# Performance work log

Hardware: AMD Instinct MI355X
Metric: run time of the kernel (lower is better)

## Reference

```python
import jax, jax.numpy as jnp
import numpy as np

C = 256
CQK = C // 8  # 32


def setup_inputs() -> dict:
    key = jax.random.key(0)
    ks = jax.random.split(key, 7)
    x = jax.random.normal(ks[0], (4, C, 64, 64), dtype=jnp.float32)
    s = 1.0 / np.sqrt(C)
    Wq = jax.random.normal(ks[1], (CQK, C), dtype=jnp.float32) * s
    bq = jnp.zeros((CQK,), dtype=jnp.float32)
    Wk = jax.random.normal(ks[2], (CQK, C), dtype=jnp.float32) * s
    bk = jnp.zeros((CQK,), dtype=jnp.float32)
    Wv = jax.random.normal(ks[3], (C, C), dtype=jnp.float32) * s
    bv = jnp.zeros((C,), dtype=jnp.float32)
    return {"x": x, "Wq": Wq, "bq": bq, "Wk": Wk, "bk": bk, "Wv": Wv, "bv": bv}


def reference(x, Wq, bq, Wk, bk, Wv, bv):
    B, Cc, H, W = x.shape
    xf = x.reshape(B, Cc, H * W)  # [B, C, HW]
    # 1x1 convs == per-pixel linear projections over channels
    q = jnp.einsum('oc,bcn->bno', Wq, xf) + bq          # [B, HW, C//8]
    k = jnp.einsum('oc,bcn->bon', Wk, xf) + bk[:, None]  # [B, C//8, HW]
    v = jnp.einsum('oc,bcn->bno', Wv, xf) + bv          # [B, HW, C]
    attn = jax.nn.softmax(jnp.einsum('bnd,bdm->bnm', q, k), axis=-1)  # [B, HW, HW]
    out = jnp.einsum('bnm,bmc->bnc', attn, v)           # [B, HW, C]
    return out.transpose(0, 2, 1).reshape(B, Cc, H, W)
```

## Files before the change

### kernel.cpp

```cpp
#include <hip/hip_runtime.h>
#include <hip/hip_bf16.h>


#define N_PIX 4096
#define DQK   32
#define CCH   256
#define LOG2E 1.44269504088896f

typedef __attribute__((ext_vector_type(8))) _Float16 f16x8;
typedef __attribute__((ext_vector_type(4))) _Float16 f16x4;
typedef __attribute__((ext_vector_type(2))) _Float16 f16x2;
typedef __attribute__((ext_vector_type(8))) short    bf16x8;
typedef __attribute__((ext_vector_type(4))) short    bf16x4;
typedef __attribute__((ext_vector_type(4))) float    f32x4;

__device__ inline void barrier_lds() {
    asm volatile("" ::: "memory");
    __builtin_amdgcn_s_waitcnt(0xc07f);
    __builtin_amdgcn_s_barrier();
    asm volatile("" ::: "memory");
}

__device__ inline short bf16bits(float f) {
    __hip_bfloat16 h = __float2bfloat16(f);
    return *(short*)&h;
}

__global__ __launch_bounds__(256) void wpack_kernel(
    const float* __restrict__ Wq, const float* __restrict__ Wk,
    const float* __restrict__ Wv, _Float16* __restrict__ Wp)
{
    const int tid   = threadIdx.x;
    const int wflat = blockIdx.x * 4 + (tid >> 6);
    const int lane  = tid & 63;
    const int L15   = lane & 15;
    const int quad  = lane >> 4;
    const int mt    = wflat >> 3;
    const int ks    = wflat & 7;
    const int m0    = mt * 16;

    const float* Wsrc; int row; float scale = 1.f;
    if (m0 < 32)      { Wsrc = Wq; row = m0 + L15;      scale = LOG2E; }
    else if (m0 < 64) { Wsrc = Wk; row = m0 - 32 + L15; }
    else              { Wsrc = Wv; row = m0 - 64 + L15; }

    const float* p = Wsrc + (size_t)row * 256 + ks * 32 + quad * 8;
    f16x8 h;
    #pragma unroll
    for (int j = 0; j < 8; ++j) h[j] = (_Float16)(p[j] * scale);
    *(f16x8*)(Wp + ((size_t)wflat * 64 + lane) * 8) = h;
}

__global__ __launch_bounds__(512, 4) void qkv_kernel(
    const float* __restrict__ x, const _Float16* __restrict__ Wp,
    const float* __restrict__ bq, const float* __restrict__ bk,
    const float* __restrict__ bv,
    _Float16* __restrict__ qo, _Float16* __restrict__ ko,
    __hip_bfloat16* __restrict__ vp)
{
    __shared__ alignas(16) unsigned char shraw[256 * 40 * 2];
    _Float16       (*xT)[264] = (_Float16 (*)[264])shraw;
    __hip_bfloat16 (*vst)[40] = (__hip_bfloat16 (*)[40])shraw;

    const int idx = blockIdx.x;
    const int b   = (idx & 7) >> 1;
    const int n0  = (((idx >> 3) << 1) | (idx & 1)) * 32;
    const int tid = threadIdx.x;

    {
        const float* xb = x + (size_t)b * CCH * N_PIX;
        float4 ld[2][2];
        int c2s[2], n4s[2];
        #pragma unroll
        for (int pass = 0; pass < 2; ++pass) {
            const int flat = pass * 512 + tid;
            c2s[pass] = (flat >> 3) * 2;
            n4s[pass] = (flat & 7) * 4;
            ld[pass][0] = *(const float4*)(xb + (size_t)c2s[pass]       * N_PIX + n0 + n4s[pass]);
            ld[pass][1] = *(const float4*)(xb + (size_t)(c2s[pass] + 1) * N_PIX + n0 + n4s[pass]);
        }
        #pragma unroll
        for (int pass = 0; pass < 2; ++pass) {
            const float a[4] = {ld[pass][0].x, ld[pass][0].y, ld[pass][0].z, ld[pass][0].w};
            const float c[4] = {ld[pass][1].x, ld[pass][1].y, ld[pass][1].z, ld[pass][1].w};
            #pragma unroll
            for (int i = 0; i < 4; ++i)
                *(f16x2*)(&xT[n4s[pass] + i][c2s[pass]]) =
                    (f16x2){(_Float16)a[i], (_Float16)c[i]};
        }
    }
    __syncthreads();

    const int lane = tid & 63;
    const int wid  = tid >> 6;
    const int L15  = lane & 15;
    const int quad = lane >> 4;
    const int nf   = wid & 1;
    const int mtg  = wid >> 1;

    const f32x4 fz = {0.f, 0.f, 0.f, 0.f};
    f32x4 acc[5];
    #pragma unroll
    for (int mt = 0; mt < 5; ++mt) acc[mt] = fz;

    const _Float16* wpw = Wp + ((size_t)(mtg * 5) * 8 * 64 + lane) * 8;

    #pragma unroll
    for (int ks = 0; ks < 8; ++ks) {
        const f16x8 bfr = *(const f16x8*)(&xT[nf * 16 + L15][ks * 32 + quad * 8]);
        #pragma unroll
        for (int mt = 0; mt < 5; ++mt) {
            const f16x8 afr = *(const f16x8*)(wpw + (size_t)(mt * 8 + ks) * 512);
            acc[mt] = __builtin_amdgcn_mfma_f32_16x16x32_f16(afr, bfr, acc[mt], 0, 0, 0);
        }
    }

    const int np = nf * 16 + L15;
    const int n  = n0 + np;
    #pragma unroll
    for (int mt = 0; mt < 5; ++mt) {
        const int m0 = (mtg * 5 + mt) * 16;
        const f32x4 a = acc[mt];
        if (m0 < 32) {
            const int mr = m0 + quad * 4;
            f16x4 h;
            #pragma unroll
            for (int r = 0; r < 4; ++r) h[r] = (_Float16)(a[r] + bq[mr + r] * LOG2E);
            *(f16x4*)(qo + ((size_t)b * N_PIX + n) * DQK + mr) = h;
        } else if (m0 < 64) {
            const int mr = m0 - 32 + quad * 4;
            f16x4 h;
            #pragma unroll
            for (int r = 0; r < 4; ++r) h[r] = (_Float16)(a[r] + bk[mr + r]);
            *(f16x4*)(ko + ((size_t)b * N_PIX + n) * DQK + mr) = h;
        }
    }

    __syncthreads();

    #pragma unroll
    for (int mt = 0; mt < 5; ++mt) {
        const int m0 = (mtg * 5 + mt) * 16;
        if (m0 >= 64) {
            const int c = m0 - 64 + quad * 4;
            #pragma unroll
            for (int r = 0; r < 4; ++r)
                vst[c + r][np] = __float2bfloat16(acc[mt][r] + bv[c + r]);
        }
    }
    __syncthreads();

    {
        __hip_bfloat16* vpb = vp + (size_t)b * 2048 * 512 + (size_t)((n0 >> 5) * 16) * 512;
        #pragma unroll
        for (int s = 0; s < 2; ++s) {
            const int slot = s * 512 + tid;
            const int cg16 = slot >> 6;
            const int ln   = slot & 63;
            const int qd   = ln >> 4;
            const int l15  = ln & 15;
            const bf16x8 val = *(const bf16x8*)(&vst[cg16 * 16 + l15][qd * 8]);
            *(bf16x8*)(vpb + ((size_t)cg16 * 64 + ln) * 8) = val;
        }
    }
}


#define ATTN_BODY(J, KR, VR, PSRD, DO_S)                                          \
  {                                                                               \
    const bool dos_ = (DO_S);                                                     \
    f32x4 s_ = fz;                                                                \
    if (dos_) s_ = __builtin_amdgcn_mfma_f32_16x16x32_f16(KR, aq, fz, 0, 0, 0);   \
                        \
    {                                                                             \
      const _Float16* kt_ = kb + (size_t)(((J) + 3) & 63) * (64 * DQK);           \
      KR = *(const f16x8*)(kt_ + koff);                                           \
    }                                                                             \
                                                          \
    _Pragma("unroll")                                                             \
    for (int qq_ = 0; qq_ < 2; ++qq_) {                                           \
      _Pragma("unroll")                                                           \
      for (int kk_ = 0; kk_ < 2; ++kk_) {                                         \
        const bf16x8 ap_ = *(const bf16x8*)(                                      \
            &Ps[PSRD][(qp * 2 + qq_) * 16 + L15][kk_ * 32 + quad * 8]);           \
        oacc[qq_][0] = __builtin_amdgcn_mfma_f32_16x16x32_bf16(                   \
            ap_, VR[kk_][0], oacc[qq_][0], 0, 0, 0);                              \
        oacc[qq_][1] = __builtin_amdgcn_mfma_f32_16x16x32_bf16(                   \
            ap_, VR[kk_][1], oacc[qq_][1], 0, 0, 0);                              \
      }                                                                           \
    }                                                                             \
                                                     \
    {                                                                             \
      const __hip_bfloat16* vt_ = vb + (size_t)(((J) + 2) & 63) * (2 * 16 * 512); \
      _Pragma("unroll")                                                           \
      for (int kk_ = 0; kk_ < 2; ++kk_)                                           \
        _Pragma("unroll")                                                         \
        for (int cf_ = 0; cf_ < 2; ++cf_)                                         \
          VR[kk_][cf_] = *(const bf16x8*)(vt_ + voff0 + kk_ * 8192 + cf_ * 512);  \
    }                                                                             \
                                          \
    if (dos_) {                                                                   \
      bf16x4 pk_;                                                                 \
      _Pragma("unroll")                                                           \
      for (int r_ = 0; r_ < 4; ++r_) {                                            \
        const float p_ = exp2f(s_[r_]);                                           \
        psum += p_;                                                               \
        pk_[r_] = bf16bits(p_);                                                   \
      }                                                                           \
      *(bf16x4*)(&Ps[(PSRD) ^ 1][qt * 16 + L15][kt * 16 + quad * 4]) = pk_;       \
    }                                                                             \
    barrier_lds();                                                                \
  }

__global__ __launch_bounds__(1024, 1) void attn_kernel(
    const _Float16* __restrict__ qg,
    const _Float16* __restrict__ kg,
    const __hip_bfloat16* __restrict__ vp,
    float* __restrict__ out)
{
    __shared__ alignas(16) __hip_bfloat16 Ps[2][64][72];
    __shared__ float lsum[4][4][16];

    const int idx  = blockIdx.x;
    const int b    = (idx & 7) >> 1;
    const int n0   = (((idx >> 3) << 1) | (idx & 1)) * 64;
    const int tid  = threadIdx.x;
    const int wid  = tid >> 6;
    const int lane = tid & 63;
    const int L15  = lane & 15;
    const int quad = lane >> 4;
    const int qt   = wid & 3;
    const int kt   = wid >> 2;
    const int qp   = wid & 1;
    const int cg   = wid >> 1;
    const int c0   = cg * 32;

    const f32x4 fz = {0.f, 0.f, 0.f, 0.f};

    const f16x8 aq = *(const f16x8*)(qg + ((size_t)b * N_PIX + n0 + qt * 16 + L15) * DQK + quad * 8);

    f32x4 oacc[2][2];
    #pragma unroll
    for (int qq = 0; qq < 2; ++qq)
        #pragma unroll
        for (int cf = 0; cf < 2; ++cf) oacc[qq][cf] = fz;
    float psum = 0.f;

    const _Float16* kb = kg + (size_t)b * N_PIX * DQK;
    const int koff  = (kt * 16 + L15) * DQK + quad * 8;
    const __hip_bfloat16* vb = vp + (size_t)b * 2048 * 512;
    const int voff0 = lane * 8 + cg * 2 * 512;

    f16x8 kA = *(const f16x8*)(kb + (size_t)1 * 64 * DQK + koff);
    f16x8 kB = *(const f16x8*)(kb + (size_t)2 * 64 * DQK + koff);
    bf16x8 vA[2][2], vB[2][2];
    #pragma unroll
    for (int kk = 0; kk < 2; ++kk)
        #pragma unroll
        for (int cf = 0; cf < 2; ++cf) {
            vA[kk][cf] = *(const bf16x8*)(vb +                    voff0 + kk * 8192 + cf * 512);
            vB[kk][cf] = *(const bf16x8*)(vb + (size_t)16384 +    voff0 + kk * 8192 + cf * 512);
        }
    {
        const f16x8 k0f = *(const f16x8*)(kb + koff);
        const f32x4 s = __builtin_amdgcn_mfma_f32_16x16x32_f16(k0f, aq, fz, 0, 0, 0);
        bf16x4 pk;
        #pragma unroll
        for (int r = 0; r < 4; ++r) { const float p = exp2f(s[r]); psum += p; pk[r] = bf16bits(p); }
        *(bf16x4*)(&Ps[0][qt * 16 + L15][kt * 16 + quad * 4]) = pk;
    }
    barrier_lds();

    for (int it = 0; it < 64; it += 2) {
        ATTN_BODY(it,     kA, vA, 0, true);
        ATTN_BODY(it + 1, kB, vB, 1, it < 62);
    }

    psum += __shfl_xor(psum, 16, 64);
    psum += __shfl_xor(psum, 32, 64);
    if (quad == 0) lsum[qt][kt][L15] = psum;
    __syncthreads();

    float* ob = out + (size_t)b * CCH * N_PIX;
    #pragma unroll
    for (int qq = 0; qq < 2; ++qq) {
        const int qtile = qp * 2 + qq;
        float inv_l[4];
        #pragma unroll
        for (int r = 0; r < 4; ++r) {
            const int q = quad * 4 + r;
            inv_l[r] = 1.f / (lsum[qtile][0][q] + lsum[qtile][1][q] +
                              lsum[qtile][2][q] + lsum[qtile][3][q]);
        }
        #pragma unroll
        for (int cf = 0; cf < 2; ++cf) {
            const int c = c0 + cf * 16 + L15;
            f32x4 o;
            #pragma unroll
            for (int r = 0; r < 4; ++r) o[r] = oacc[qq][cf][r] * inv_l[r];
            *(f32x4*)(ob + (size_t)c * N_PIX + n0 + qtile * 16 + quad * 4) = o;
        }
    }
}

extern "C" void kernel_launch(void* const* d_in, const int* in_sizes, int n_in,
                              void* d_out, int out_size, void* d_ws, size_t ws_size,
                              hipStream_t stream) {
    (void)in_sizes; (void)n_in; (void)out_size; (void)ws_size;
    const float* x  = (const float*)d_in[0];
    const float* Wq = (const float*)d_in[1];
    const float* bq = (const float*)d_in[2];
    const float* Wk = (const float*)d_in[3];
    const float* bk = (const float*)d_in[4];
    const float* Wv = (const float*)d_in[5];
    const float* bv = (const float*)d_in[6];

    _Float16* qb = (_Float16*)d_ws;
    _Float16* kb = qb + (size_t)4 * N_PIX * DQK;
    __hip_bfloat16* vpk = (__hip_bfloat16*)(kb + (size_t)4 * N_PIX * DQK);
    _Float16* wp = (_Float16*)(vpk + (size_t)4 * 2048 * 512);
    float* outp = (float*)d_out;

    wpack_kernel<<<40, 256, 0, stream>>>(Wq, Wk, Wv, wp);
    qkv_kernel<<<512, 512, 0, stream>>>(x, wp, bq, bk, bv, qb, kb, vpk);
    attn_kernel<<<256, 1024, 0, stream>>>(qb, kb, vpk, outp);
}
```

Before: 146.7 us.

## Halve attention query tile per block, swizzle P tile in LDS, pack bf16 conversion

The attention kernel now handles 32 queries per 512-thread block instead of 64 queries per 1024-thread block. This doubles the grid to 512 blocks and allows several blocks per CU through the new launch bounds. The P tile in LDS gets an XOR swizzle on the column index to reduce bank conflicts. Probabilities are converted to bf16 with a packed v_cvt_pk_bf16_f32 instruction. In exchange, each K/V tile is reused across fewer queries, so global K/V traffic roughly doubles.

New measurement: 147.8 us. About the same (+0.7%).

```diff
diff --git a/kernel.cpp b/kernel.cpp
--- a/kernel.cpp
+++ b/kernel.cpp
@@ -24,6 +24,12 @@
 __device__ inline short bf16bits(float f) {
     __hip_bfloat16 h = __float2bfloat16(f);
     return *(short*)&h;
+}
+
+__device__ inline unsigned cvt_pk_bf16(float lo, float hi) {
+    unsigned r;
+    asm("v_cvt_pk_bf16_f32 %0, %1, %2" : "=v"(r) : "v"(lo), "v"(hi));
+    return r;
 }
 
 __global__ __launch_bounds__(256) void wpack_kernel(
@@ -182,7 +188,7 @@
       _Pragma("unroll")                                                           \
       for (int kk_ = 0; kk_ < 2; ++kk_) {                                         \
         const bf16x8 ap_ = *(const bf16x8*)(                                      \
-            &Ps[PSRD][(qp * 2 + qq_) * 16 + L15][kk_ * 32 + quad * 8]);           \
+            &Ps[PSRD][qq_ * 16 + L15][(kk_ * 32 + quad * 8) ^ sw8]);              \
         oacc[qq_][0] = __builtin_amdgcn_mfma_f32_16x16x32_bf16(                   \
             ap_, VR[kk_][0], oacc[qq_][0], 0, 0, 0);                              \
         oacc[qq_][1] = __builtin_amdgcn_mfma_f32_16x16x32_bf16(                   \
@@ -200,40 +206,39 @@
     }                                                                             \
                                           \
     if (dos_) {                                                                   \
-      bf16x4 pk_;                                                                 \
-      _Pragma("unroll")                                                           \
-      for (int r_ = 0; r_ < 4; ++r_) {                                            \
-        const float p_ = exp2f(s_[r_]);                                           \
-        psum += p_;                                                               \
-        pk_[r_] = bf16bits(p_);                                                   \
-      }                                                                           \
-      *(bf16x4*)(&Ps[(PSRD) ^ 1][qt * 16 + L15][kt * 16 + quad * 4]) = pk_;       \
+      const float p0_ = exp2f(s_[0]), p1_ = exp2f(s_[1]);                         \
+      const float p2_ = exp2f(s_[2]), p3_ = exp2f(s_[3]);                         \
+      psum += (p0_ + p1_) + (p2_ + p3_);                                          \
+      uint2 pk_;                                                                  \
+      pk_.x = cvt_pk_bf16(p0_, p1_);                                              \
+      pk_.y = cvt_pk_bf16(p2_, p3_);                                              \
+      *(uint2*)(&Ps[(PSRD) ^ 1][qt * 16 + L15][(kt * 16 + quad * 4) ^ sw8]) = pk_;\
     }                                                                             \
     barrier_lds();                                                                \
   }
 
-__global__ __launch_bounds__(1024, 1) void attn_kernel(
+__global__ __launch_bounds__(512, 4) void attn_kernel(
     const _Float16* __restrict__ qg,
     const _Float16* __restrict__ kg,
     const __hip_bfloat16* __restrict__ vp,
     float* __restrict__ out)
 {
-    __shared__ alignas(16) __hip_bfloat16 Ps[2][64][72];
-    __shared__ float lsum[4][4][16];
+    __shared__ alignas(16) __hip_bfloat16 Ps[2][32][72];
+    __shared__ float lsum[2][4][16];
 
     const int idx  = blockIdx.x;
     const int b    = (idx & 7) >> 1;
-    const int n0   = (((idx >> 3) << 1) | (idx & 1)) * 64;
+    const int n0   = (((idx >> 3) << 1) | (idx & 1)) * 32;
     const int tid  = threadIdx.x;
     const int wid  = tid >> 6;
     const int lane = tid & 63;
     const int L15  = lane & 15;
     const int quad = lane >> 4;
-    const int qt   = wid & 3;
-    const int kt   = wid >> 2;
-    const int qp   = wid & 1;
-    const int cg   = wid >> 1;
+    const int qt   = wid & 1;
+    const int kt   = wid >> 1;
+    const int cg   = wid;
     const int c0   = cg * 32;
+    const int sw8  = ((L15 >> 3) & 1) << 3;
 
     const f32x4 fz = {0.f, 0.f, 0.f, 0.f};
 
@@ -258,16 +263,19 @@
     for (int kk = 0; kk < 2; ++kk)
         #pragma unroll
         for (int cf = 0; cf < 2; ++cf) {
-            vA[kk][cf] = *(const bf16x8*)(vb +                    voff0 + kk * 8192 + cf * 512);
-            vB[kk][cf] = *(const bf16x8*)(vb + (size_t)16384 +    voff0 + kk * 8192 + cf * 512);
+            vA[kk][cf] = *(const bf16x8*)(vb +                 voff0 + kk * 8192 + cf * 512);
+            vB[kk][cf] = *(const bf16x8*)(vb + (size_t)16384 + voff0 + kk * 8192 + cf * 512);
         }
     {
         const f16x8 k0f = *(const f16x8*)(kb + koff);
         const f32x4 s = __builtin_amdgcn_mfma_f32_16x16x32_f16(k0f, aq, fz, 0, 0, 0);
-        bf16x4 pk;
-        #pragma unroll
-        for (int r = 0; r < 4; ++r) { const float p = exp2f(s[r]); psum += p; pk[r] = bf16bits(p); }
-        *(bf16x4*)(&Ps[0][qt * 16 + L15][kt * 16 + quad * 4]) = pk;
+        const float p0 = exp2f(s[0]), p1 = exp2f(s[1]);
+        const float p2 = exp2f(s[2]), p3 = exp2f(s[3]);
+        psum += (p0 + p1) + (p2 + p3);
+        uint2 pk;
+        pk.x = cvt_pk_bf16(p0, p1);
+        pk.y = cvt_pk_bf16(p2, p3);
+        *(uint2*)(&Ps[0][qt * 16 + L15][(kt * 16 + quad * 4) ^ sw8]) = pk;
     }
     barrier_lds();
 
@@ -284,13 +292,12 @@
     float* ob = out + (size_t)b * CCH * N_PIX;
     #pragma unroll
     for (int qq = 0; qq < 2; ++qq) {
-        const int qtile = qp * 2 + qq;
         float inv_l[4];
         #pragma unroll
         for (int r = 0; r < 4; ++r) {
             const int q = quad * 4 + r;
-            inv_l[r] = 1.f / (lsum[qtile][0][q] + lsum[qtile][1][q] +
-                              lsum[qtile][2][q] + lsum[qtile][3][q]);
+            inv_l[r] = 1.f / (lsum[qq][0][q] + lsum[qq][1][q] +
+                              lsum[qq][2][q] + lsum[qq][3][q]);
         }
         #pragma unroll
         for (int cf = 0; cf < 2; ++cf) {
@@ -298,7 +305,7 @@
             f32x4 o;
             #pragma unroll
             for (int r = 0; r < 4; ++r) o[r] = oacc[qq][cf][r] * inv_l[r];
-            *(f32x4*)(ob + (size_t)c * N_PIX + n0 + qtile * 16 + quad * 4) = o;
+            *(f32x4*)(ob + (size_t)c * N_PIX + n0 + qq * 16 + quad * 4) = o;
         }
     }
 }
@@ -323,5 +330,5 @@
 
     wpack_kernel<<<40, 256, 0, stream>>>(Wq, Wk, Wv, wp);
     qkv_kernel<<<512, 512, 0, stream>>>(x, wp, bq, bk, bv, qb, kb, vpk);
-    attn_kernel<<<256, 1024, 0, stream>>>(qb, kb, vpk, outp);
-}
+    attn_kernel<<<512, 512, 0, stream>>>(qb, kb, vpk, outp);
+}
```
